# Optimization experiments

Hardware: AMD Instinct MI355X
Metric: run time of the kernel (lower is better)

Reference implementation:

```python
import jax, jax.numpy as jnp
import numpy as np

HIDDEN = 300
DEPTH = 6
ATOM_FDIM = 136
BOND_FDIM = 12
BOND_IN = ATOM_FDIM + BOND_FDIM  # 148
MAX_NB = 6
N_MOLS = 4096
ATOMS_PER_MOL = 32
N_ATOMS = N_MOLS * ATOMS_PER_MOL  # 131072
N_BONDS = 2 * N_ATOMS            # 262144 directed bonds


def setup_inputs() -> dict:
    key = jax.random.key(0)
    ks = jax.random.split(key, 11)
    fatoms = jax.random.normal(ks[0], (N_ATOMS, ATOM_FDIM), jnp.float32)
    fbonds = jax.random.normal(ks[1], (N_BONDS, BOND_IN), jnp.float32)
    agraph = jax.random.randint(ks[2], (N_ATOMS, MAX_NB), 0, N_BONDS, jnp.int32)
    bgraph = jax.random.randint(ks[3], (N_BONDS, MAX_NB), 0, N_BONDS, jnp.int32)
    # Linear weights stored pre-transposed so forward is x @ W
    W_i = jax.random.normal(ks[4], (BOND_IN, HIDDEN), jnp.float32) / np.sqrt(BOND_IN)
    W_h = jax.random.normal(ks[5], (HIDDEN, HIDDEN), jnp.float32) / np.sqrt(HIDDEN)
    W_o = jax.random.normal(ks[6], (ATOM_FDIM + HIDDEN, HIDDEN), jnp.float32) / np.sqrt(ATOM_FDIM + HIDDEN)
    b_o = jax.random.normal(ks[7], (HIDDEN,), jnp.float32) * 0.01
    W_a = jax.random.normal(ks[8], (HIDDEN, HIDDEN), jnp.float32) / np.sqrt(HIDDEN)
    W_b = jax.random.normal(ks[9], (HIDDEN, HIDDEN), jnp.float32) / np.sqrt(HIDDEN)
    b_b = jax.random.normal(ks[10], (HIDDEN,), jnp.float32) * 0.01
    return {"fatoms": fatoms, "fbonds": fbonds, "agraph": agraph, "bgraph": bgraph,
            "W_i": W_i, "W_h": W_h, "W_o": W_o, "b_o": b_o,
            "W_a": W_a, "W_b": W_b, "b_b": b_b}


def reference(fatoms, fbonds, agraph, bgraph, W_i, W_h, W_o, b_o, W_a, W_b, b_b):
    # D-MPNN bond message passing (dropout=0.0 -> identity)
    binput = fbonds @ W_i                         # [N_b, H]
    message = jax.nn.relu(binput)
    for _ in range(DEPTH - 1):
        nei = jnp.take(message, bgraph, axis=0).sum(axis=1)   # gather [N_b, MAX_NB, H] -> sum
        message = jax.nn.relu(binput + nei @ W_h)
    nei_a = jnp.take(message, agraph, axis=0).sum(axis=1)     # [N_a, H]
    atom_hiddens = jax.nn.relu(jnp.concatenate([fatoms, nei_a], axis=1) @ W_o + b_o)
    # Per-molecule self-attention pooling (fixed-size scope: ATOMS_PER_MOL atoms/mol)
    h = atom_hiddens.reshape(N_MOLS, ATOMS_PER_MOL, HIDDEN)   # [B, A, H]
    q = jnp.einsum('bah,hk->bak', h, W_a)
    att = jax.nn.softmax(jnp.einsum('bak,bck->bac', q, h), axis=-1)
    att_h = jax.nn.relu(jnp.einsum('bac,bch->bah', att, h) @ W_b + b_b)
    mol_vecs = (h + att_h).sum(axis=1) / ATOMS_PER_MOL        # [B, H]
    return mol_vecs
```

## Files before the change

kernel.cpp:

```cpp
#include <hip/hip_runtime.h>
#include <hip/hip_fp16.h>
#include <math.h>

#define HIDDEN 300
#define ATOM_FDIM 136
#define BOND_IN 148
#define MAX_NB 6
#define N_MOLS 4096
#define APM 32
#define N_ATOMS (N_MOLS*APM)
#define N_BONDS (2*N_ATOMS)

#define BK 16
#define BM 64
#define ASTR 68
#define BSTR 304

#define WT_C 304
#define WT_K 320

typedef unsigned short u16;
typedef short bf16x8 __attribute__((ext_vector_type(8)));
typedef float f32x4  __attribute__((ext_vector_type(4)));

__device__ float g_scratch[3ull * N_BONDS * HIDDEN + (size_t)N_MOLS * HIDDEN + WT_C * WT_K];

__device__ __forceinline__ u16 bf16_rne(float x) {
    unsigned u = __float_as_uint(x);
    unsigned r = (u + 0x7fffu + ((u >> 16) & 1u)) >> 16;
    return (u16)r;
}
__device__ __forceinline__ float bf16_f(u16 h) {
    return __uint_as_float(((unsigned)h) << 16);
}
__device__ __forceinline__ void st_h4(__half* p, float a, float b, float c, float d) {
    *(__half2*)(p)     = __floats2half2_rn(a, b);
    *(__half2*)(p + 2) = __floats2half2_rn(c, d);
}

__global__ __launch_bounds__(256)
void wt_prep(const float* __restrict__ W, u16* __restrict__ wt_hi, u16* __restrict__ wt_lo)
{
    const int i = blockIdx.x * 256 + threadIdx.x;
    if (i >= WT_C * WT_K) return;
    const int c = i / WT_K, k = i - c * WT_K;
    float w = (c < HIDDEN && k < HIDDEN) ? W[(size_t)k * HIDDEN + c] : 0.f;
    const u16 hi = bf16_rne(w);
    const u16 lo = bf16_rne(w - bf16_f(hi));
    wt_hi[i] = hi;
    wt_lo[i] = lo;
}

__global__ __launch_bounds__(512)
void mp_mfma(const __half* __restrict__ msg,
             const int*   __restrict__ graph,
             const u16*   __restrict__ wt_hi,
             const u16*   __restrict__ wt_lo,
             const __half* __restrict__ binput,
             __half* __restrict__ out0)
{
    __shared__ u16 Ahi[64 * 40];
    __shared__ u16 Alo[64 * 40];
    __shared__ int gx[64 * MAX_NB];

    const int tid  = threadIdx.x;
    const int row0 = blockIdx.x * 64;

    if (tid < 64 * MAX_NB) gx[tid] = graph[(size_t)row0 * MAX_NB + tid];
    __syncthreads();

    const int w  = tid >> 6;
    const int l  = tid & 63;
    const int g  = l >> 4;
    const int mr = (w & 3) * 16 + (l & 15);
    const int tbase = (w >> 2) ? 10 : 0;
    const int ntile = (w >> 2) ? 9 : 10;

    const int sr = tid >> 3;
    const int sk = (tid & 7) * 4;
    const int* sg = &gx[sr * MAX_NB];

    f32x4 acc[10];
#pragma unroll
    for (int t = 0; t < 10; ++t) acc[t] = (f32x4){0.f, 0.f, 0.f, 0.f};

    for (int k0 = 0; k0 < HIDDEN; k0 += 32) {
        const int kk = k0 + sk;
        float s0 = 0.f, s1 = 0.f, s2 = 0.f, s3 = 0.f;
#pragma unroll
        for (int j = 0; j < MAX_NB; ++j) {
            const __half2* p = (const __half2*)(msg + (size_t)sg[j] * HIDDEN + kk);
            const float2 u = __half22float2(p[0]);
            const float2 v = __half22float2(p[1]);
            s0 += u.x; s1 += u.y; s2 += v.x; s3 += v.y;
        }
        const u16 h0 = bf16_rne(s0), h1 = bf16_rne(s1), h2 = bf16_rne(s2), h3 = bf16_rne(s3);
        const u16 e0 = bf16_rne(s0 - bf16_f(h0)), e1 = bf16_rne(s1 - bf16_f(h1));
        const u16 e2 = bf16_rne(s2 - bf16_f(h2)), e3 = bf16_rne(s3 - bf16_f(h3));
        uint2 ph, pl;
        ph.x = (unsigned)h0 | ((unsigned)h1 << 16);
        ph.y = (unsigned)h2 | ((unsigned)h3 << 16);
        pl.x = (unsigned)e0 | ((unsigned)e1 << 16);
        pl.y = (unsigned)e2 | ((unsigned)e3 << 16);
        *(uint2*)&Ahi[sr * 40 + sk] = ph;
        *(uint2*)&Alo[sr * 40 + sk] = pl;
        __syncthreads();

        const bf16x8 ahi = *(const bf16x8*)&Ahi[mr * 40 + 8 * g];
        const bf16x8 alo = *(const bf16x8*)&Alo[mr * 40 + 8 * g];
        const int kb = k0 + 8 * g;

#pragma unroll
        for (int t = 0; t < 10; ++t) {
            if (t < ntile) {
                const int cn = 16 * (tbase + t) + (l & 15);
                const bf16x8 bhi = *(const bf16x8*)&wt_hi[(size_t)cn * WT_K + kb];
                const bf16x8 blo = *(const bf16x8*)&wt_lo[(size_t)cn * WT_K + kb];
                acc[t] = __builtin_amdgcn_mfma_f32_16x16x32_bf16(ahi, bhi, acc[t], 0, 0, 0);
                acc[t] = __builtin_amdgcn_mfma_f32_16x16x32_bf16(ahi, blo, acc[t], 0, 0, 0);
                acc[t] = __builtin_amdgcn_mfma_f32_16x16x32_bf16(alo, bhi, acc[t], 0, 0, 0);
            }
        }
        __syncthreads();
    }

#pragma unroll
    for (int t = 0; t < 10; ++t) {
        if (t < ntile) {
            const int col = 16 * (tbase + t) + (l & 15);
            if (col < HIDDEN) {
#pragma unroll
                for (int j = 0; j < 4; ++j) {
                    const size_t off = (size_t)(row0 + (w & 3) * 16 + 4 * g + j) * HIDDEN + col;
                    out0[off] = __float2half(fmaxf(__half2float(binput[off]) + acc[t][j], 0.f));
                }
            }
        }
    }
}

template<int MODE>
__global__ __launch_bounds__(512)
void gemm_fused(const float* __restrict__ Adense, int lda,
                const void*  __restrict__ msgv,
                const int*   __restrict__ graph,
                const float* __restrict__ W,
                const float* __restrict__ bias,
                const float* __restrict__ hsum,
                float* __restrict__ out0,
                float* __restrict__ out1,
                int K)
{
    __shared__ float As[BK * ASTR];
    __shared__ float Bs[BK * BSTR];
    __shared__ int   gx[BM * MAX_NB];

    const int tid  = threadIdx.x;
    const int wave = tid >> 6;
    const int lane = tid & 63;
    const int row0 = blockIdx.x * BM;
    const int c0   = 4 * lane;
    const bool has4 = (lane < HIDDEN - 256);
    const int  c4   = has4 ? (256 + lane) : 256;

    if (MODE == 2) {
        if (tid < BM * MAX_NB) gx[tid] = graph[(size_t)row0 * MAX_NB + tid];
        __syncthreads();
    }

    float acc[8][5];
#pragma unroll
    for (int r = 0; r < 8; ++r)
#pragma unroll
        for (int c = 0; c < 5; ++c) acc[r][c] = 0.f;

    const int nk = (K + BK - 1) / BK;
    for (int kt = 0; kt < nk; ++kt) {
        const int k0 = kt * BK;
        for (int i = tid; i < BK * 300; i += 512) {
            const int kk = i / 300;
            const int col = i - kk * 300;
            const int k = k0 + kk;
            Bs[kk * BSTR + col] = (k < K) ? W[(size_t)k * HIDDEN + col] : 0.f;
        }
        for (int i = tid; i < BK * BM; i += 512) {
            const int r  = i >> 4;
            const int kk = i & 15;
            const int k  = k0 + kk;
            float v = 0.f;
            if (MODE == 0 || MODE == 3 || MODE == 4) {
                if (k < K) v = Adense[(size_t)(row0 + r) * lda + k];
            } else {
                if (k < ATOM_FDIM) {
                    v = Adense[(size_t)(row0 + r) * lda + k];
                } else if (k < K) {
                    const int kc = k - ATOM_FDIM;
                    const __half* mh = (const __half*)msgv;
#pragma unroll
                    for (int j = 0; j < MAX_NB; ++j)
                        v += __half2float(mh[(size_t)gx[r * MAX_NB + j] * HIDDEN + kc]);
                }
            }
            As[kk * ASTR + r] = v;
        }
        __syncthreads();
#pragma unroll
        for (int kk = 0; kk < BK; ++kk) {
            const float4 bq = *(const float4*)&Bs[kk * BSTR + c0];
            const float  b4 = Bs[kk * BSTR + c4];
            const float4 a0 = *(const float4*)&As[kk * ASTR + wave * 8];
            const float4 a1 = *(const float4*)&As[kk * ASTR + wave * 8 + 4];
            const float ar8[8] = {a0.x, a0.y, a0.z, a0.w, a1.x, a1.y, a1.z, a1.w};
#pragma unroll
            for (int r = 0; r < 8; ++r) {
                acc[r][0] = fmaf(ar8[r], bq.x, acc[r][0]);
                acc[r][1] = fmaf(ar8[r], bq.y, acc[r][1]);
                acc[r][2] = fmaf(ar8[r], bq.z, acc[r][2]);
                acc[r][3] = fmaf(ar8[r], bq.w, acc[r][3]);
                acc[r][4] = fmaf(ar8[r], b4,   acc[r][4]);
            }
        }
        __syncthreads();
    }

    if (MODE == 4) {
        const float4 bqv = *(const float4*)&bias[c0];
        const float  b4v = bias[c4];
        float s0 = 0, s1 = 0, s2 = 0, s3 = 0, s4 = 0;
#pragma unroll
        for (int r = 0; r < 8; ++r) {
            s0 += fmaxf(acc[r][0] + bqv.x, 0.f);
            s1 += fmaxf(acc[r][1] + bqv.y, 0.f);
            s2 += fmaxf(acc[r][2] + bqv.z, 0.f);
            s3 += fmaxf(acc[r][3] + bqv.w, 0.f);
            s4 += fmaxf(acc[r][4] + b4v,   0.f);
        }
        float* wsum = Bs;
        *(float4*)&wsum[wave * BSTR + c0] = make_float4(s0, s1, s2, s3);
        if (has4) wsum[wave * BSTR + c4] = s4;
        __syncthreads();
        const int m0 = blockIdx.x * 2;
        for (int t = tid; t < 2 * HIDDEN; t += 512) {
            const int m = t / HIDDEN, col = t - m * HIDDEN;
            const float v = wsum[(4 * m + 0) * BSTR + col] + wsum[(4 * m + 1) * BSTR + col]
                          + wsum[(4 * m + 2) * BSTR + col] + wsum[(4 * m + 3) * BSTR + col]
                          + hsum[(size_t)(m0 + m) * HIDDEN + col];
            out0[(size_t)(m0 + m) * HIDDEN + col] = v * (1.f / 32.f);
        }
        return;
    }

#pragma unroll
    for (int r = 0; r < 8; ++r) {
        const size_t off = (size_t)(row0 + wave * 8 + r) * HIDDEN;
        float4 v = make_float4(acc[r][0], acc[r][1], acc[r][2], acc[r][3]);
        float v4 = acc[r][4];
        if (MODE == 0) {
            __half* o0 = (__half*)out0;
            __half* o1 = (__half*)out1;
            st_h4(&o0[off + c0], v.x, v.y, v.z, v.w);
            if (has4) o0[off + c4] = __float2half(v4);
            st_h4(&o1[off + c0], fmaxf(v.x,0.f), fmaxf(v.y,0.f), fmaxf(v.z,0.f), fmaxf(v.w,0.f));
            if (has4) o1[off + c4] = __float2half(fmaxf(v4, 0.f));
        } else if (MODE == 2) {
            const float4 bb = *(const float4*)&bias[c0];
            float4 rv = make_float4(fmaxf(v.x+bb.x,0.f), fmaxf(v.y+bb.y,0.f),
                                    fmaxf(v.z+bb.z,0.f), fmaxf(v.w+bb.w,0.f));
            *(float4*)&out0[off + c0] = rv;
            if (has4) out0[off + c4] = fmaxf(v4 + bias[c4], 0.f);
        } else {
            *(float4*)&out0[off + c0] = v;
            if (has4) out0[off + c4] = v4;
        }
    }
}

#define HSTR 320

__device__ __forceinline__ int hsw(int a, int c4u) {
    return a * HSTR + ((c4u ^ (a & 7)) << 2);
}

__global__ __launch_bounds__(512)
void attn_mid(const float* __restrict__ atom_h,
              const float* __restrict__ q_all,
              float* __restrict__ P_all,
              float* __restrict__ hsum)
{
    __shared__ float hs[APM * HSTR];
    __shared__ float qs[APM * HIDDEN];
    __shared__ float att[APM][33];

    const int tid  = threadIdx.x;
    const int wave = tid >> 6;
    const int lane = tid & 63;
    const int mol  = blockIdx.x;
    const float* hb = atom_h + (size_t)mol * APM * HIDDEN;
    const float* qb = q_all  + (size_t)mol * APM * HIDDEN;

    for (int j = tid; j < APM * 75; j += 512) {
        const int a = j / 75, c4u = j - a * 75;
        *(float4*)&hs[hsw(a, c4u)] = *(const float4*)&hb[(size_t)a * HIDDEN + 4 * c4u];
    }
    for (int j = tid; j < APM * 75; j += 512)
        *(float4*)&qs[4 * j] = *(const float4*)&qb[4 * j];
    __syncthreads();

    {
        const int a = tid >> 5, b = tid & 31;
        float s0 = 0.f, s1 = 0.f;
        for (int t = 0; t < 75; ++t) {
            const float4 hv = *(const float4*)&hs[hsw(b, t)];
            const float4 q0 = *(const float4*)&qs[a * HIDDEN + 4 * t];
            const float4 q1 = *(const float4*)&qs[(a + 16) * HIDDEN + 4 * t];
            s0 = fmaf(q0.x, hv.x, fmaf(q0.y, hv.y, fmaf(q0.z, hv.z, fmaf(q0.w, hv.w, s0))));
            s1 = fmaf(q1.x, hv.x, fmaf(q1.y, hv.y, fmaf(q1.z, hv.z, fmaf(q1.w, hv.w, s1))));
        }
        att[a][b] = s0;
        att[a + 16][b] = s1;
    }
    __syncthreads();

    if (tid < APM) {
        float m = -3.4e38f;
#pragma unroll 4
        for (int b = 0; b < APM; ++b) m = fmaxf(m, att[tid][b]);
        float s = 0.f;
#pragma unroll 4
        for (int b = 0; b < APM; ++b) { const float e = __expf(att[tid][b] - m); att[tid][b] = e; s += e; }
        const float inv = 1.f / s;
#pragma unroll 4
        for (int b = 0; b < APM; ++b) att[tid][b] *= inv;
    }
    __syncthreads();

    {
        const int r0 = wave * 4;
        const int c0 = 4 * lane;
        const bool has4 = (lane < 44);
        const int c4u = 64 + (lane >> 2), c4r = lane & 3;
        float4 p[4];
        float  p4[4];
#pragma unroll
        for (int r = 0; r < 4; ++r) { p[r] = make_float4(0,0,0,0); p4[r] = 0.f; }
#pragma unroll 4
        for (int b = 0; b < APM; ++b) {
            const float4 hv = *(const float4*)&hs[hsw(b, lane)];
            const float  h4 = hs[hsw(b, c4u) + c4r];
#pragma unroll
            for (int r = 0; r < 4; ++r) {
                const float av = att[r0 + r][b];
                p[r].x = fmaf(av, hv.x, p[r].x);
                p[r].y = fmaf(av, hv.y, p[r].y);
                p[r].z = fmaf(av, hv.z, p[r].z);
                p[r].w = fmaf(av, hv.w, p[r].w);
                p4[r]  = fmaf(av, h4,   p4[r]);
            }
        }
#pragma unroll
        for (int r = 0; r < 4; ++r) {
            const size_t off = ((size_t)mol * APM + r0 + r) * HIDDEN;
            *(float4*)&P_all[off + c0] = p[r];
            if (has4) P_all[off + 256 + lane] = p4[r];
        }
    }

    if (tid < HIDDEN) {
        const int c4u = tid >> 2, cr = tid & 3;
        float s = 0.f;
#pragma unroll 4
        for (int a = 0; a < APM; ++a) s += hs[hsw(a, c4u) + cr];
        hsum[(size_t)mol * HIDDEN + tid] = s;
    }
}

extern "C" void kernel_launch(void* const* d_in, const int* in_sizes, int n_in,
                              void* d_out, int out_size, void* d_ws, size_t ws_size,
                              hipStream_t stream)
{
    const float* fatoms = (const float*)d_in[0];
    const float* fbonds = (const float*)d_in[1];
    const int*   agraph = (const int*)d_in[2];
    const int*   bgraph = (const int*)d_in[3];
    const float* W_i    = (const float*)d_in[4];
    const float* W_h    = (const float*)d_in[5];
    const float* W_o    = (const float*)d_in[6];
    const float* b_o    = (const float*)d_in[7];
    const float* W_a    = (const float*)d_in[8];
    const float* W_b    = (const float*)d_in[9];
    const float* b_b    = (const float*)d_in[10];
    float* out = (float*)d_out;

    const size_t WB = (size_t)N_BONDS * HIDDEN;
    const size_t WA = (size_t)N_ATOMS * HIDDEN;
    const size_t need = (3 * WB / 2 + 3 * WA + (size_t)N_MOLS * HIDDEN + WT_C * WT_K) * sizeof(float);
    float* base;
    if (ws_size >= need) {
        base = (float*)d_ws;
    } else {
        void* p = nullptr;
        (void)hipGetSymbolAddress(&p, HIP_SYMBOL(g_scratch));
        base = (float*)p;
    }
    __half* binput_h = (__half*)base;
    __half* msgA     = (__half*)(base + WB / 2);
    __half* msgB     = (__half*)(base + WB);
    float*  atom_h   = base + 3 * WB / 2;
    float*  q_all    = atom_h + WA;
    float*  P_all    = q_all + WA;
    float*  hsum     = P_all + WA;
    u16*    wt_hi    = (u16*)(hsum + (size_t)N_MOLS * HIDDEN);
    u16*    wt_lo    = wt_hi + WT_C * WT_K;

    const dim3 blk(512);

    wt_prep<<<(WT_C * WT_K + 255) / 256, dim3(256), 0, stream>>>(W_h, wt_hi, wt_lo);

    gemm_fused<0><<<N_BONDS / BM, blk, 0, stream>>>(
        fbonds, BOND_IN, nullptr, nullptr, W_i, nullptr, nullptr,
        (float*)binput_h, (float*)msgA, BOND_IN);

    const __half* cur = msgA;
    __half* nxt = msgB;
    for (int it = 0; it < 5; ++it) {
        mp_mfma<<<N_BONDS / 64, blk, 0, stream>>>(
            cur, bgraph, wt_hi, wt_lo, binput_h, nxt);
        __half* t = nxt; nxt = (__half*)cur; cur = t;
    }

    gemm_fused<2><<<N_ATOMS / BM, blk, 0, stream>>>(
        fatoms, ATOM_FDIM, (const void*)cur, agraph, W_o, b_o, nullptr,
        atom_h, nullptr, ATOM_FDIM + HIDDEN);

    gemm_fused<3><<<N_ATOMS / BM, blk, 0, stream>>>(
        atom_h, HIDDEN, nullptr, nullptr, W_a, nullptr, nullptr,
        q_all, nullptr, HIDDEN);

    attn_mid<<<N_MOLS, dim3(512), 0, stream>>>(atom_h, q_all, P_all, hsum);

    gemm_fused<4><<<N_ATOMS / BM, blk, 0, stream>>>(
        P_all, HIDDEN, nullptr, nullptr, W_b, b_b, hsum,
        out, nullptr, HIDDEN);
}
```

Measured before the change: 6.973 ms.

## Gather full neighbor-sum tile into LDS upfront in message-passing MFMA kernel

The message-passing kernel now gathers and sums the neighbor messages for a 32-row tile across the whole hidden dimension in one phase, using wider 8-half loads, and stores hi/lo bf16 splits in LDS. The previous version had a gather/sync/MFMA/sync loop per 32-wide K chunk; the new MFMA loop runs without block barriers. The block is re-tiled to 32 rows, with 8 waves split as 2 M-tiles by 4 N-groups, and launch bounds ask for 4 blocks per CU. The binput epilogue read uses a nontemporal load. The trade-off is a larger LDS footprint per block and twice as many blocks, each re-reading the weight tiles.

```diff
diff --git a/kernel.cpp b/kernel.cpp
--- a/kernel.cpp
+++ b/kernel.cpp
@@ -18,6 +18,9 @@
 
 #define WT_C 304
 #define WT_K 320
+
+#define MP_BM 32
+#define MP_STR 328
 
 typedef unsigned short u16;
 typedef short bf16x8 __attribute__((ext_vector_type(8)));
@@ -51,7 +54,7 @@
     wt_lo[i] = lo;
 }
 
-__global__ __launch_bounds__(512)
+__global__ __launch_bounds__(512, 4)
 void mp_mfma(const __half* __restrict__ msg,
              const int*   __restrict__ graph,
              const u16*   __restrict__ wt_hi,
@@ -59,61 +62,88 @@
              const __half* __restrict__ binput,
              __half* __restrict__ out0)
 {
-    __shared__ u16 Ahi[64 * 40];
-    __shared__ u16 Alo[64 * 40];
-    __shared__ int gx[64 * MAX_NB];
+    __shared__ u16 Ahi[MP_BM * MP_STR];
+    __shared__ u16 Alo[MP_BM * MP_STR];
+    __shared__ int gx[MP_BM * MAX_NB];
 
     const int tid  = threadIdx.x;
-    const int row0 = blockIdx.x * 64;
-
-    if (tid < 64 * MAX_NB) gx[tid] = graph[(size_t)row0 * MAX_NB + tid];
+    const int row0 = blockIdx.x * MP_BM;
+
+    if (tid < MP_BM * MAX_NB) gx[tid] = graph[(size_t)row0 * MAX_NB + tid];
+    __syncthreads();
+
+    const int sr = tid >> 4;
+    const int sc = (tid & 15) * 8;
+    const int* sg = &gx[sr * MAX_NB];
+
+    if ((tid & 15) < 3) {
+        const int kp = 304 + (tid & 15) * 8;
+        *(uint4*)&Ahi[sr * MP_STR + kp] = make_uint4(0, 0, 0, 0);
+        *(uint4*)&Alo[sr * MP_STR + kp] = make_uint4(0, 0, 0, 0);
+    }
+
+#pragma unroll
+    for (int p = 0; p < 3; ++p) {
+        const int kk = sc + 128 * p;
+        if (kk < 304) {
+            float s[8];
+#pragma unroll
+            for (int e = 0; e < 8; ++e) s[e] = 0.f;
+            const bool hi_ok = (kk + 4 < HIDDEN);
+#pragma unroll
+            for (int j = 0; j < MAX_NB; ++j) {
+                const __half* rp = msg + (size_t)sg[j] * HIDDEN + kk;
+                const uint2 q0 = *(const uint2*)rp;
+                const uint2 q1 = hi_ok ? *(const uint2*)(rp + 4) : make_uint2(0u, 0u);
+                const float2 a0 = __half22float2(*(const __half2*)&q0.x);
+                const float2 a1 = __half22float2(*(const __half2*)&q0.y);
+                const float2 a2 = __half22float2(*(const __half2*)&q1.x);
+                const float2 a3 = __half22float2(*(const __half2*)&q1.y);
+                s[0] += a0.x; s[1] += a0.y; s[2] += a1.x; s[3] += a1.y;
+                s[4] += a2.x; s[5] += a2.y; s[6] += a3.x; s[7] += a3.y;
+            }
+            u16 h[8], e[8];
+#pragma unroll
+            for (int q = 0; q < 8; ++q) {
+                h[q] = bf16_rne(s[q]);
+                e[q] = bf16_rne(s[q] - bf16_f(h[q]));
+            }
+            uint4 ph, pl;
+            ph.x = (unsigned)h[0] | ((unsigned)h[1] << 16);
+            ph.y = (unsigned)h[2] | ((unsigned)h[3] << 16);
+            ph.z = (unsigned)h[4] | ((unsigned)h[5] << 16);
+            ph.w = (unsigned)h[6] | ((unsigned)h[7] << 16);
+            pl.x = (unsigned)e[0] | ((unsigned)e[1] << 16);
+            pl.y = (unsigned)e[2] | ((unsigned)e[3] << 16);
+            pl.z = (unsigned)e[4] | ((unsigned)e[5] << 16);
+            pl.w = (unsigned)e[6] | ((unsigned)e[7] << 16);
+            *(uint4*)&Ahi[sr * MP_STR + kk] = ph;
+            *(uint4*)&Alo[sr * MP_STR + kk] = pl;
+        }
+    }
     __syncthreads();
 
     const int w  = tid >> 6;
     const int l  = tid & 63;
     const int g  = l >> 4;
-    const int mr = (w & 3) * 16 + (l & 15);
-    const int tbase = (w >> 2) ? 10 : 0;
-    const int ntile = (w >> 2) ? 9 : 10;
-
-    const int sr = tid >> 3;
-    const int sk = (tid & 7) * 4;
-    const int* sg = &gx[sr * MAX_NB];
-
-    f32x4 acc[10];
-#pragma unroll
-    for (int t = 0; t < 10; ++t) acc[t] = (f32x4){0.f, 0.f, 0.f, 0.f};
+    const int mt = w & 1;
+    const int ng = w >> 1;
+    const int nbase  = ng * 5;
+    const int ntiles = (ng < 3) ? 5 : 4;
+    const int mr = mt * 16 + (l & 15);
+
+    f32x4 acc[5];
+#pragma unroll
+    for (int t = 0; t < 5; ++t) acc[t] = (f32x4){0.f, 0.f, 0.f, 0.f};
 
     for (int k0 = 0; k0 < HIDDEN; k0 += 32) {
-        const int kk = k0 + sk;
-        float s0 = 0.f, s1 = 0.f, s2 = 0.f, s3 = 0.f;
-#pragma unroll
-        for (int j = 0; j < MAX_NB; ++j) {
-            const __half2* p = (const __half2*)(msg + (size_t)sg[j] * HIDDEN + kk);
-            const float2 u = __half22float2(p[0]);
-            const float2 v = __half22float2(p[1]);
-            s0 += u.x; s1 += u.y; s2 += v.x; s3 += v.y;
-        }
-        const u16 h0 = bf16_rne(s0), h1 = bf16_rne(s1), h2 = bf16_rne(s2), h3 = bf16_rne(s3);
-        const u16 e0 = bf16_rne(s0 - bf16_f(h0)), e1 = bf16_rne(s1 - bf16_f(h1));
-        const u16 e2 = bf16_rne(s2 - bf16_f(h2)), e3 = bf16_rne(s3 - bf16_f(h3));
-        uint2 ph, pl;
-        ph.x = (unsigned)h0 | ((unsigned)h1 << 16);
-        ph.y = (unsigned)h2 | ((unsigned)h3 << 16);
-        pl.x = (unsigned)e0 | ((unsigned)e1 << 16);
-        pl.y = (unsigned)e2 | ((unsigned)e3 << 16);
-        *(uint2*)&Ahi[sr * 40 + sk] = ph;
-        *(uint2*)&Alo[sr * 40 + sk] = pl;
-        __syncthreads();
-
-        const bf16x8 ahi = *(const bf16x8*)&Ahi[mr * 40 + 8 * g];
-        const bf16x8 alo = *(const bf16x8*)&Alo[mr * 40 + 8 * g];
         const int kb = k0 + 8 * g;
-
-#pragma unroll
-        for (int t = 0; t < 10; ++t) {
-            if (t < ntile) {
-                const int cn = 16 * (tbase + t) + (l & 15);
+        const bf16x8 ahi = *(const bf16x8*)&Ahi[mr * MP_STR + kb];
+        const bf16x8 alo = *(const bf16x8*)&Alo[mr * MP_STR + kb];
+#pragma unroll
+        for (int t = 0; t < 5; ++t) {
+            if (t < ntiles) {
+                const int cn = 16 * (nbase + t) + (l & 15);
                 const bf16x8 bhi = *(const bf16x8*)&wt_hi[(size_t)cn * WT_K + kb];
                 const bf16x8 blo = *(const bf16x8*)&wt_lo[(size_t)cn * WT_K + kb];
                 acc[t] = __builtin_amdgcn_mfma_f32_16x16x32_bf16(ahi, bhi, acc[t], 0, 0, 0);
@@ -121,18 +151,20 @@
                 acc[t] = __builtin_amdgcn_mfma_f32_16x16x32_bf16(alo, bhi, acc[t], 0, 0, 0);
             }
         }
-        __syncthreads();
-    }
-
-#pragma unroll
-    for (int t = 0; t < 10; ++t) {
-        if (t < ntile) {
-            const int col = 16 * (tbase + t) + (l & 15);
+    }
+
+    const u16* bin_u = (const u16*)binput;
+#pragma unroll
+    for (int t = 0; t < 5; ++t) {
+        if (t < ntiles) {
+            const int col = 16 * (nbase + t) + (l & 15);
             if (col < HIDDEN) {
 #pragma unroll
                 for (int j = 0; j < 4; ++j) {
-                    const size_t off = (size_t)(row0 + (w & 3) * 16 + 4 * g + j) * HIDDEN + col;
-                    out0[off] = __float2half(fmaxf(__half2float(binput[off]) + acc[t][j], 0.f));
+                    const size_t off = (size_t)(row0 + mt * 16 + 4 * g + j) * HIDDEN + col;
+                    const u16 raw = __builtin_nontemporal_load(bin_u + off);
+                    const float bi = __half2float(__ushort_as_half(raw));
+                    out0[off] = __float2half(fmaxf(bi + acc[t][j], 0.f));
                 }
             }
         }
@@ -423,7 +455,7 @@
     const __half* cur = msgA;
     __half* nxt = msgB;
     for (int it = 0; it < 5; ++it) {
-        mp_mfma<<<N_BONDS / 64, blk, 0, stream>>>(
+        mp_mfma<<<N_BONDS / MP_BM, blk, 0, stream>>>(
             cur, bgraph, wt_hi, wt_lo, binput_h, nxt);
         __half* t = nxt; nxt = (__half*)cur; cur = t;
     }
```

Result: slower. 7.428 ms (+6.5%).
